# Kernel tuning notes

Hardware: AMD Instinct MI355X
Metric: run time of the kernel (lower is better)

The kernel has to match this reference:

```python
import jax, jax.numpy as jnp
import numpy as np

D_MODEL = 1024
N_HEADS = 16
HEAD_DIM = D_MODEL // N_HEADS


def setup_inputs() -> dict:
    key = jax.random.key(0)
    k1, k2, k3 = jax.random.split(key, 3)
    scale = 0.02
    x = jax.random.normal(k1, (2, 2048, D_MODEL), dtype=jnp.float32)
    w_qkv = jax.random.normal(k2, (D_MODEL, 3 * D_MODEL), dtype=jnp.float32) * scale
    b_qkv = jnp.zeros((3 * D_MODEL,), dtype=jnp.float32)
    w_proj = jax.random.normal(k3, (D_MODEL, D_MODEL), dtype=jnp.float32) * scale
    b_proj = jnp.zeros((D_MODEL,), dtype=jnp.float32)
    return {"x": x, "w_qkv": w_qkv, "b_qkv": b_qkv, "w_proj": w_proj, "b_proj": b_proj}


def reference(x, w_qkv, b_qkv, w_proj, b_proj):
    bsz, seq_len, d_model = x.shape
    qkv = x @ w_qkv + b_qkv  # [B,S,3D]
    q, k, v = jnp.split(qkv, 3, axis=-1)
    # [B,S,D] -> [B,H,S,hd]
    def to_heads(t):
        return t.reshape(bsz, seq_len, N_HEADS, HEAD_DIM).transpose(0, 2, 1, 3)
    q, k, v = to_heads(q), to_heads(k), to_heads(v)
    scores = jnp.einsum("bhqd,bhkd->bhqk", q, k) / jnp.sqrt(jnp.float32(HEAD_DIM))
    causal = jnp.triu(jnp.ones((seq_len, seq_len), dtype=bool), k=1)
    scores = jnp.where(causal, -jnp.inf, scores)
    attn = jax.nn.softmax(scores, axis=-1)
    out = jnp.einsum("bhqk,bhkd->bhqd", attn, v)  # [B,H,S,hd]
    out = out.transpose(0, 2, 1, 3).reshape(bsz, seq_len, d_model)
    return out @ w_proj + b_proj
```

## Files before the change

### kernel.cpp

```cpp
#include <hip/hip_runtime.h>
#include <hip/hip_bf16.h>

#define D_MODEL 1024
#define SEQ     2048
#define NH      16
#define HD      64
#define M_TOK   4096
#define THREE_D 3072

using bf16x8 = __bf16 __attribute__((ext_vector_type(8)));
using bf16x4 = __bf16 __attribute__((ext_vector_type(4)));
using f32x4  = float  __attribute__((ext_vector_type(4)));

typedef __attribute__((address_space(3))) uint32_t lds_u32;
typedef const __attribute__((address_space(1))) uint32_t glb_u32;

__global__ __launch_bounds__(256) void cast_kernel(const float* __restrict__ in,
                                                   __bf16* __restrict__ out, int n4) {
  int i = blockIdx.x * 256 + threadIdx.x;
  if (i < n4) {
    float4 f = reinterpret_cast<const float4*>(in)[i];
    bf16x4 o;
    o[0] = (__bf16)f.x; o[1] = (__bf16)f.y; o[2] = (__bf16)f.z; o[3] = (__bf16)f.w;
    reinterpret_cast<bf16x4*>(out)[i] = o;
  }
}

__global__ __launch_bounds__(256) void transpose_cast(const float* __restrict__ in,
                                                      __bf16* __restrict__ out, int R, int C) {
  __shared__ float tile[64][65];
  int c0 = blockIdx.x * 64, r0 = blockIdx.y * 64;
  int tx = threadIdx.x & 63, ty = threadIdx.x >> 6;
#pragma unroll
  for (int i = 0; i < 16; ++i) {
    int r = ty + i * 4;
    tile[r][tx] = in[(size_t)(r0 + r) * C + c0 + tx];
  }
  __syncthreads();
#pragma unroll
  for (int i = 0; i < 16; ++i) {
    int r = ty + i * 4;
    out[(size_t)(c0 + r) * R + r0 + tx] = (__bf16)tile[tx][r];
  }
}

__global__ __launch_bounds__(256, 3) void gemm_qkv(const __bf16* __restrict__ A,
                                                   const __bf16* __restrict__ BT,
                                                   const float* __restrict__ bias,
                                                   __bf16* __restrict__ qb, __bf16* __restrict__ kb,
                                                   __bf16* __restrict__ vb) {
  __shared__ __bf16 As[128 * 32];
  __shared__ __bf16 Bs[128 * 32];
  const int Kdim = D_MODEL;
  const int tid  = threadIdx.x;
  const int lane = tid & 63, wave = tid >> 6;
  const int lr = lane & 15, lg = lane >> 4;
  const int wm = (wave >> 1) * 64, wn = (wave & 1) * 64;
  const int m0 = blockIdx.y * 128, n0 = blockIdx.x * 128;
  const int srow = tid >> 2, scol = (tid & 3) * 8;

  f32x4 acc[4][4] = {};

  const __bf16* aSrc = A  + (size_t)(m0 + srow) * Kdim + scol;
  const __bf16* bSrc = BT + (size_t)(n0 + srow) * Kdim + scol;
  __bf16* aDst = As + wave * 512;
  __bf16* bDst = Bs + wave * 512;

  for (int k0 = 0; k0 < Kdim; k0 += 32) {
    __syncthreads();
    __builtin_amdgcn_global_load_lds((glb_u32*)(aSrc + k0),              (lds_u32*)aDst,          16, 0, 0);
    __builtin_amdgcn_global_load_lds((glb_u32*)(aSrc + 64 * Kdim + k0), (lds_u32*)(aDst + 2048), 16, 0, 0);
    __builtin_amdgcn_global_load_lds((glb_u32*)(bSrc + k0),              (lds_u32*)bDst,          16, 0, 0);
    __builtin_amdgcn_global_load_lds((glb_u32*)(bSrc + 64 * Kdim + k0), (lds_u32*)(bDst + 2048), 16, 0, 0);
    asm volatile("s_waitcnt vmcnt(0)" ::: "memory");
    __syncthreads();

    bf16x8 af[4], bfv[4];
#pragma unroll
    for (int i = 0; i < 4; ++i) af[i]  = *reinterpret_cast<const bf16x8*>(&As[(wm + i * 16 + lr) * 32 + lg * 8]);
#pragma unroll
    for (int j = 0; j < 4; ++j) bfv[j] = *reinterpret_cast<const bf16x8*>(&Bs[(wn + j * 16 + lr) * 32 + lg * 8]);
#pragma unroll
    for (int i = 0; i < 4; ++i)
#pragma unroll
      for (int j = 0; j < 4; ++j)
        acc[i][j] = __builtin_amdgcn_mfma_f32_16x16x32_bf16(af[i], bfv[j], acc[i][j], 0, 0, 0);
  }

#pragma unroll
  for (int i = 0; i < 4; ++i) {
#pragma unroll
    for (int j = 0; j < 4; ++j) {
      const int gc = n0 + wn + j * 16 + lr;
      const float bv = bias[gc];
      const int t = gc >> 10, rem = gc & 1023;
      const int h = rem >> 6, d = rem & 63;
#pragma unroll
      for (int ii = 0; ii < 4; ++ii) {
        const int gr = m0 + wm + i * 16 + lg * 4 + ii;
        const float val = acc[i][j][ii] + bv;
        const int b = gr >> 11, s = gr & 2047;
        if (t == 0) {
          qb[(((size_t)(b * NH + h)) * SEQ + s) * HD + d] = (__bf16)(val * 0.125f);
        } else if (t == 1) {
          kb[(((size_t)(b * NH + h)) * SEQ + s) * HD + d] = (__bf16)val;
        } else {
          vb[(((size_t)(b * NH + h)) * HD + d) * SEQ + s] = (__bf16)val;
        }
      }
    }
  }
}

__global__ __launch_bounds__(256, 4) void gemm_proj(const __bf16* __restrict__ A,
                                                    const __bf16* __restrict__ BT,
                                                    const float* __restrict__ bias,
                                                    float* __restrict__ fout) {
  __shared__ __bf16 As[64 * 32];
  __shared__ __bf16 Bs[128 * 32];
  const int Kdim = D_MODEL;
  const int tid  = threadIdx.x;
  const int lane = tid & 63, wave = tid >> 6;
  const int lr = lane & 15, lg = lane >> 4;
  const int wm = (wave >> 1) * 32, wn = (wave & 1) * 64;
  const int n0 = blockIdx.x * 128, m0 = blockIdx.y * 64;
  const int srow = tid >> 2, scol = (tid & 3) * 8;

  f32x4 acc[2][4] = {};

  const __bf16* aSrc = A  + (size_t)(m0 + srow) * Kdim + scol;
  const __bf16* bSrc = BT + (size_t)(n0 + srow) * Kdim + scol;
  __bf16* aDst = As + wave * 512;
  __bf16* bDst = Bs + wave * 512;

  for (int k0 = 0; k0 < Kdim; k0 += 32) {
    __syncthreads();
    __builtin_amdgcn_global_load_lds((glb_u32*)(aSrc + k0),              (lds_u32*)aDst,          16, 0, 0);
    __builtin_amdgcn_global_load_lds((glb_u32*)(bSrc + k0),              (lds_u32*)bDst,          16, 0, 0);
    __builtin_amdgcn_global_load_lds((glb_u32*)(bSrc + 64 * Kdim + k0), (lds_u32*)(bDst + 2048), 16, 0, 0);
    asm volatile("s_waitcnt vmcnt(0)" ::: "memory");
    __syncthreads();

    bf16x8 af[2], bfv[4];
#pragma unroll
    for (int i = 0; i < 2; ++i) af[i]  = *reinterpret_cast<const bf16x8*>(&As[(wm + i * 16 + lr) * 32 + lg * 8]);
#pragma unroll
    for (int j = 0; j < 4; ++j) bfv[j] = *reinterpret_cast<const bf16x8*>(&Bs[(wn + j * 16 + lr) * 32 + lg * 8]);
#pragma unroll
    for (int i = 0; i < 2; ++i)
#pragma unroll
      for (int j = 0; j < 4; ++j)
        acc[i][j] = __builtin_amdgcn_mfma_f32_16x16x32_bf16(af[i], bfv[j], acc[i][j], 0, 0, 0);
  }

#pragma unroll
  for (int i = 0; i < 2; ++i) {
#pragma unroll
    for (int j = 0; j < 4; ++j) {
      const int gc = n0 + wn + j * 16 + lr;
      const float bv = bias[gc];
#pragma unroll
      for (int ii = 0; ii < 4; ++ii) {
        const int gr = m0 + wm + i * 16 + lg * 4 + ii;
        fout[(size_t)gr * D_MODEL + gc] = acc[i][j][ii] + bv;
      }
    }
  }
}

__global__ __launch_bounds__(256, 4) void attn_kernel(const __bf16* __restrict__ Q,
                                                      const __bf16* __restrict__ K,
                                                      const __bf16* __restrict__ VT,
                                                      __bf16* __restrict__ AO) {
  __shared__ __bf16 Kb[2][64 * 64];
  __shared__ __bf16 Vb[2][64 * 64];
  __shared__ __bf16 Ps[4][16 * 64];

  const int tid  = threadIdx.x;
  const int lane = tid & 63, wave = tid >> 6;
  const int lr = lane & 15, lg = lane >> 4;

  const int f  = blockIdx.x;
  const int c  = f & 7;
  const int u  = f >> 3;
  const int bh = c * 4 + (u & 3);
  const int s2 = u >> 2, grp = s2 >> 3, r = s2 & 7;
  const int qblk = (grp == 0) ? (31 - r) : (grp == 1) ? r : (grp == 2) ? (39 - s2) : (s2 - 16);

  const int q0 = qblk * 64 + wave * 16;
  const size_t base = (size_t)bh * SEQ * HD;
  const char* Kg  = (const char*)(K + base);
  const char* VTg = (const char*)(VT + base);

  bf16x8 qf[2];
#pragma unroll
  for (int kc = 0; kc < 2; ++kc)
    qf[kc] = *reinterpret_cast<const bf16x8*>(Q + base + (size_t)(q0 + lr) * HD + kc * 32 + lg * 8);

  float lrun[4] = {0.f, 0.f, 0.f, 0.f};
  f32x4 o[4] = {};

  const int nt = qblk + 1;
  const int nmaxF = (wave | 1) + 1;

  auto stage = [&](int bufp, int t) {
    const int k0 = t * 64;
#pragma unroll
    for (int p = 0; p < 2; ++p) {
      const int row = wave * 16 + p * 8 + (lane >> 3);
      {
        const int srcOff = (k0 + row) * 128 + (((lane & 7) ^ (row & 7)) << 4);
        __builtin_amdgcn_global_load_lds((glb_u32*)(Kg + srcOff),
                                         (lds_u32*)&Kb[bufp][(wave * 16 + p * 8) * 64], 16, 0, 0);
      }
      {
        const int srcOff = row * 4096 + k0 * 2 + (((lane & 7) ^ (row & 7)) << 4);
        __builtin_amdgcn_global_load_lds((glb_u32*)(VTg + srcOff),
                                         (lds_u32*)&Vb[bufp][(wave * 16 + p * 8) * 64], 16, 0, 0);
      }
    }
  };

  stage(0, 0);
  asm volatile("s_waitcnt vmcnt(0)" ::: "memory");
  __syncthreads();

  for (int t = 0; t < nt; ++t) {
    const int p = t & 1;
    const int k0 = t * 64;
    const bool last = (t == nt - 1);
    const int nmax = last ? nmaxF : 4;
    const int kcmax = nmax >> 1;

    if (t + 1 < nt) stage(p ^ 1, t + 1);

    const __bf16* Kt = Kb[p];
    const __bf16* Vt = Vb[p];

    f32x4 s[4] = {};
#pragma unroll
    for (int kc = 0; kc < 2; ++kc) {
#pragma unroll
      for (int n = 0; n < 4; ++n)
        if (n < nmax) {
          bf16x8 kf = *reinterpret_cast<const bf16x8*>(
              &Kt[(n * 16 + lr) * 64 + (((kc * 4 + lg) ^ (lr & 7)) << 3)]);
          s[n] = __builtin_amdgcn_mfma_f32_16x16x32_bf16(qf[kc], kf, s[n], 0, 0, 0);
        }
    }

    if (last) {
#pragma unroll
      for (int n = 0; n < 4; ++n)
        if (n < nmax)
#pragma unroll
          for (int ii = 0; ii < 4; ++ii) {
            int qg = q0 + lg * 4 + ii;
            int kg = k0 + n * 16 + lr;
            if (kg > qg) s[n][ii] = -__builtin_inff();
          }
    }

#pragma unroll
    for (int n = 0; n < 4; ++n)
      if (n < nmax)
#pragma unroll
        for (int ii = 0; ii < 4; ++ii) {
          float pv = __expf(s[n][ii]);
          lrun[ii] += pv;
          const int row = lg * 4 + ii;
          Ps[wave][row * 64 + (((n * 2 + (lr >> 3)) ^ (row & 7)) << 3) + (lr & 7)] = (__bf16)pv;
        }

#pragma unroll
    for (int kc = 0; kc < 2; ++kc)
      if (kc < kcmax) {
        bf16x8 pa = *reinterpret_cast<const bf16x8*>(
            &Ps[wave][lr * 64 + (((kc * 4 + lg) ^ (lr & 7)) << 3)]);
#pragma unroll
        for (int nd = 0; nd < 4; ++nd) {
          bf16x8 vf = *reinterpret_cast<const bf16x8*>(
              &Vt[(nd * 16 + lr) * 64 + (((kc * 4 + lg) ^ (lr & 7)) << 3)]);
          o[nd] = __builtin_amdgcn_mfma_f32_16x16x32_bf16(pa, vf, o[nd], 0, 0, 0);
        }
      }

    asm volatile("s_waitcnt vmcnt(0)" ::: "memory");
    __syncthreads();
  }

#pragma unroll
  for (int off = 1; off <= 8; off <<= 1)
#pragma unroll
    for (int ii = 0; ii < 4; ++ii) lrun[ii] += __shfl_xor(lrun[ii], off, 64);

  const int b = bh >> 4, h = bh & 15;
  float rl[4];
#pragma unroll
  for (int ii = 0; ii < 4; ++ii) rl[ii] = 1.f / lrun[ii];
#pragma unroll
  for (int nd = 0; nd < 4; ++nd)
#pragma unroll
    for (int ii = 0; ii < 4; ++ii) {
      int row = q0 + lg * 4 + ii;
      AO[((size_t)(b * SEQ) + row) * D_MODEL + h * HD + nd * 16 + lr] = (__bf16)(o[nd][ii] * rl[ii]);
    }
}

extern "C" void kernel_launch(void* const* d_in, const int* in_sizes, int n_in,
                              void* d_out, int out_size, void* d_ws, size_t ws_size,
                              hipStream_t stream) {
  const float* x      = (const float*)d_in[0];
  const float* w_qkv  = (const float*)d_in[1];
  const float* b_qkv  = (const float*)d_in[2];
  const float* w_proj = (const float*)d_in[3];
  const float* b_proj = (const float*)d_in[4];
  float* out = (float*)d_out;

  char* ws = (char*)d_ws;
  __bf16* xb     = (__bf16*)(ws);
  __bf16* wqkvT  = (__bf16*)(ws + 8388608);
  __bf16* wprojT = (__bf16*)(ws + 14680064);
  __bf16* qb     = (__bf16*)(ws + 16777216);
  __bf16* kb     = (__bf16*)(ws + 25165824);
  __bf16* vtb    = (__bf16*)(ws + 33554432);
  __bf16* ao     = (__bf16*)(ws + 41943040);

  cast_kernel<<<4096, 256, 0, stream>>>(x, xb, M_TOK * D_MODEL / 4);
  transpose_cast<<<dim3(THREE_D / 64, D_MODEL / 64), 256, 0, stream>>>(w_qkv, wqkvT, D_MODEL, THREE_D);
  transpose_cast<<<dim3(D_MODEL / 64, D_MODEL / 64), 256, 0, stream>>>(w_proj, wprojT, D_MODEL, D_MODEL);

  gemm_qkv<<<dim3(THREE_D / 128, M_TOK / 128), 256, 0, stream>>>(
      xb, wqkvT, b_qkv, qb, kb, vtb);

  attn_kernel<<<1024, 256, 0, stream>>>(qb, kb, vtb, ao);

  gemm_proj<<<dim3(D_MODEL / 128, M_TOK / 64), 256, 0, stream>>>(
      ao, wprojT, b_proj, out);
}
```

Before: 114.8 us.

## Double-buffer GEMM LDS tiles and remap blocks for XCD-aware locality

Both projection GEMMs now use two LDS buffers per operand and issue the global-to-LDS loads for the next K-slice before computing the current one, waiting only on the older loads. The goal is to hide global memory latency behind the MFMA work. Launches change to 1D grids whose block index is swizzled so that blocks dispatched to the same XCD (blockIdx mod 8) cover neighbouring tiles, improving L2 reuse. The cost is twice the LDS per block, which may lower occupancy, plus an extra barrier per iteration. A no-op wave check left in gemm_proj's staging lambda has no effect.

```diff
diff --git a/kernel.cpp b/kernel.cpp
--- a/kernel.cpp
+++ b/kernel.cpp
@@ -49,42 +49,56 @@
                                                    const float* __restrict__ bias,
                                                    __bf16* __restrict__ qb, __bf16* __restrict__ kb,
                                                    __bf16* __restrict__ vb) {
-  __shared__ __bf16 As[128 * 32];
-  __shared__ __bf16 Bs[128 * 32];
+  __shared__ __bf16 As[2][128 * 32];
+  __shared__ __bf16 Bs[2][128 * 32];
   const int Kdim = D_MODEL;
   const int tid  = threadIdx.x;
   const int lane = tid & 63, wave = tid >> 6;
   const int lr = lane & 15, lg = lane >> 4;
   const int wm = (wave >> 1) * 64, wn = (wave & 1) * 64;
-  const int m0 = blockIdx.y * 128, n0 = blockIdx.x * 128;
+
+  const int f   = blockIdx.x;
+  const int swz = (f & 7) * 96 + (f >> 3);
+  const int m0  = (swz / 24) * 128, n0 = (swz % 24) * 128;
+
   const int srow = tid >> 2, scol = (tid & 3) * 8;
 
   f32x4 acc[4][4] = {};
 
   const __bf16* aSrc = A  + (size_t)(m0 + srow) * Kdim + scol;
   const __bf16* bSrc = BT + (size_t)(n0 + srow) * Kdim + scol;
-  __bf16* aDst = As + wave * 512;
-  __bf16* bDst = Bs + wave * 512;
-
-  for (int k0 = 0; k0 < Kdim; k0 += 32) {
-    __syncthreads();
-    __builtin_amdgcn_global_load_lds((glb_u32*)(aSrc + k0),              (lds_u32*)aDst,          16, 0, 0);
-    __builtin_amdgcn_global_load_lds((glb_u32*)(aSrc + 64 * Kdim + k0), (lds_u32*)(aDst + 2048), 16, 0, 0);
-    __builtin_amdgcn_global_load_lds((glb_u32*)(bSrc + k0),              (lds_u32*)bDst,          16, 0, 0);
-    __builtin_amdgcn_global_load_lds((glb_u32*)(bSrc + 64 * Kdim + k0), (lds_u32*)(bDst + 2048), 16, 0, 0);
-    asm volatile("s_waitcnt vmcnt(0)" ::: "memory");
+
+  auto stage = [&](int p, int k0) {
+    __builtin_amdgcn_global_load_lds((glb_u32*)(aSrc + k0),              (lds_u32*)(As[p] + wave * 512),        16, 0, 0);
+    __builtin_amdgcn_global_load_lds((glb_u32*)(aSrc + 64 * Kdim + k0), (lds_u32*)(As[p] + wave * 512 + 2048), 16, 0, 0);
+    __builtin_amdgcn_global_load_lds((glb_u32*)(bSrc + k0),              (lds_u32*)(Bs[p] + wave * 512),        16, 0, 0);
+    __builtin_amdgcn_global_load_lds((glb_u32*)(bSrc + 64 * Kdim + k0), (lds_u32*)(Bs[p] + wave * 512 + 2048), 16, 0, 0);
+  };
+
+  stage(0, 0);
+  const int nk = Kdim / 32;
+  for (int kk = 0; kk < nk; ++kk) {
+    const int cur = kk & 1;
+    if (kk + 1 < nk) {
+      stage(cur ^ 1, (kk + 1) * 32);
+      asm volatile("s_waitcnt vmcnt(4)" ::: "memory");
+    } else {
+      asm volatile("s_waitcnt vmcnt(0)" ::: "memory");
+    }
     __syncthreads();
 
     bf16x8 af[4], bfv[4];
 #pragma unroll
-    for (int i = 0; i < 4; ++i) af[i]  = *reinterpret_cast<const bf16x8*>(&As[(wm + i * 16 + lr) * 32 + lg * 8]);
-#pragma unroll
-    for (int j = 0; j < 4; ++j) bfv[j] = *reinterpret_cast<const bf16x8*>(&Bs[(wn + j * 16 + lr) * 32 + lg * 8]);
+    for (int i = 0; i < 4; ++i) af[i]  = *reinterpret_cast<const bf16x8*>(&As[cur][(wm + i * 16 + lr) * 32 + lg * 8]);
+#pragma unroll
+    for (int j = 0; j < 4; ++j) bfv[j] = *reinterpret_cast<const bf16x8*>(&Bs[cur][(wn + j * 16 + lr) * 32 + lg * 8]);
 #pragma unroll
     for (int i = 0; i < 4; ++i)
 #pragma unroll
       for (int j = 0; j < 4; ++j)
         acc[i][j] = __builtin_amdgcn_mfma_f32_16x16x32_bf16(af[i], bfv[j], acc[i][j], 0, 0, 0);
+
+    __syncthreads();
   }
 
 #pragma unroll
@@ -116,41 +130,57 @@
                                                     const __bf16* __restrict__ BT,
                                                     const float* __restrict__ bias,
                                                     float* __restrict__ fout) {
-  __shared__ __bf16 As[64 * 32];
-  __shared__ __bf16 Bs[128 * 32];
+  __shared__ __bf16 As[2][64 * 32];
+  __shared__ __bf16 Bs[2][128 * 32];
   const int Kdim = D_MODEL;
   const int tid  = threadIdx.x;
   const int lane = tid & 63, wave = tid >> 6;
   const int lr = lane & 15, lg = lane >> 4;
   const int wm = (wave >> 1) * 32, wn = (wave & 1) * 64;
-  const int n0 = blockIdx.x * 128, m0 = blockIdx.y * 64;
+
+  const int f   = blockIdx.x;
+  const int swz = (f & 7) * 64 + (f >> 3);
+  const int n0  = (swz & 7) * 128, m0 = (swz >> 3) * 64;
+
   const int srow = tid >> 2, scol = (tid & 3) * 8;
 
   f32x4 acc[2][4] = {};
 
   const __bf16* aSrc = A  + (size_t)(m0 + srow) * Kdim + scol;
   const __bf16* bSrc = BT + (size_t)(n0 + srow) * Kdim + scol;
-  __bf16* aDst = As + wave * 512;
-  __bf16* bDst = Bs + wave * 512;
-
-  for (int k0 = 0; k0 < Kdim; k0 += 32) {
-    __syncthreads();
-    __builtin_amdgcn_global_load_lds((glb_u32*)(aSrc + k0),              (lds_u32*)aDst,          16, 0, 0);
-    __builtin_amdgcn_global_load_lds((glb_u32*)(bSrc + k0),              (lds_u32*)bDst,          16, 0, 0);
-    __builtin_amdgcn_global_load_lds((glb_u32*)(bSrc + 64 * Kdim + k0), (lds_u32*)(bDst + 2048), 16, 0, 0);
-    asm volatile("s_waitcnt vmcnt(0)" ::: "memory");
+
+  auto stage = [&](int p, int k0) {
+    if (wave == 0 || wave == 1)
+      ;
+    __builtin_amdgcn_global_load_lds((glb_u32*)(aSrc + k0),              (lds_u32*)(As[p] + wave * 512),        16, 0, 0);
+    __builtin_amdgcn_global_load_lds((glb_u32*)(bSrc + k0),              (lds_u32*)(Bs[p] + wave * 512),        16, 0, 0);
+    __builtin_amdgcn_global_load_lds((glb_u32*)(bSrc + 64 * Kdim + k0), (lds_u32*)(Bs[p] + wave * 512 + 2048), 16, 0, 0);
+  };
+
+  stage(0, 0);
+  const int nk = Kdim / 32;
+  for (int kk = 0; kk < nk; ++kk) {
+    const int cur = kk & 1;
+    if (kk + 1 < nk) {
+      stage(cur ^ 1, (kk + 1) * 32);
+      asm volatile("s_waitcnt vmcnt(3)" ::: "memory");
+    } else {
+      asm volatile("s_waitcnt vmcnt(0)" ::: "memory");
+    }
     __syncthreads();
 
     bf16x8 af[2], bfv[4];
 #pragma unroll
-    for (int i = 0; i < 2; ++i) af[i]  = *reinterpret_cast<const bf16x8*>(&As[(wm + i * 16 + lr) * 32 + lg * 8]);
-#pragma unroll
-    for (int j = 0; j < 4; ++j) bfv[j] = *reinterpret_cast<const bf16x8*>(&Bs[(wn + j * 16 + lr) * 32 + lg * 8]);
+    for (int i = 0; i < 2; ++i) af[i]  = *reinterpret_cast<const bf16x8*>(&As[cur][(wm + i * 16 + lr) * 32 + lg * 8]);
+#pragma unroll
+    for (int j = 0; j < 4; ++j) bfv[j] = *reinterpret_cast<const bf16x8*>(&Bs[cur][(wn + j * 16 + lr) * 32 + lg * 8]);
 #pragma unroll
     for (int i = 0; i < 2; ++i)
 #pragma unroll
       for (int j = 0; j < 4; ++j)
         acc[i][j] = __builtin_amdgcn_mfma_f32_16x16x32_bf16(af[i], bfv[j], acc[i][j], 0, 0, 0);
+
+    __syncthreads();
   }
 
 #pragma unroll
@@ -330,11 +360,9 @@
   transpose_cast<<<dim3(THREE_D / 64, D_MODEL / 64), 256, 0, stream>>>(w_qkv, wqkvT, D_MODEL, THREE_D);
   transpose_cast<<<dim3(D_MODEL / 64, D_MODEL / 64), 256, 0, stream>>>(w_proj, wprojT, D_MODEL, D_MODEL);
 
-  gemm_qkv<<<dim3(THREE_D / 128, M_TOK / 128), 256, 0, stream>>>(
-      xb, wqkvT, b_qkv, qb, kb, vtb);
+  gemm_qkv<<<768, 256, 0, stream>>>(xb, wqkvT, b_qkv, qb, kb, vtb);
 
   attn_kernel<<<1024, 256, 0, stream>>>(qb, kb, vtb, ao);
 
-  gemm_proj<<<dim3(D_MODEL / 128, M_TOK / 64), 256, 0, stream>>>(
-      ao, wprojT, b_proj, out);
-}
+  gemm_proj<<<512, 256, 0, stream>>>(ao, wprojT, b_proj, out);
+}
```

Result: no change. 115.4 us (+0.5%).
